# Optimization experiments

Hardware: AMD Instinct MI355X
Metric: run time of the kernel (lower is better)

The kernel has to match this reference:

```python
import jax, jax.numpy as jnp
import numpy as np

B, S, H = 4, 1024, 1024
NH, HD = 16, 64            # heads, head_dim (H = NH*HD)
E, K, I = 8, 2, 2048       # experts, top_k, moe_intermediate_size
CAP_FACTOR = 2.0
EPS_RMS = 1e-6
EPS_LN = 1e-6
SCALE = HD ** -0.5


def setup_inputs() -> dict:
    key = jax.random.key(0)
    ks = jax.random.split(key, 12)
    std = 0.02
    causal = jnp.where(jnp.tril(jnp.ones((S, S), bool)), 0.0, -1e9).astype(jnp.float32)
    return {
        "hidden_states": jax.random.normal(ks[0], (B, S, H), jnp.float32),
        "attn_mask": causal[None, None],                       # [1,1,S,S] additive
        "qw": jax.random.normal(ks[1], (H, H), jnp.float32) * std,
        "qb": jnp.zeros((H,), jnp.float32),
        "kw": jax.random.normal(ks[2], (H, H), jnp.float32) * std,
        "kb": jnp.zeros((H,), jnp.float32),
        "vw": jax.random.normal(ks[3], (H, H), jnp.float32) * std,
        "vb": jnp.zeros((H,), jnp.float32),
        "ow": jax.random.normal(ks[4], (H, H), jnp.float32) * std,
        "ob": jnp.zeros((H,), jnp.float32),
        "rms_w": jnp.ones((H,), jnp.float32),
        "gate_w": jax.random.normal(ks[5], (E, H), jnp.float32) * std,
        "w1": jax.random.normal(ks[6], (E, H, I), jnp.float32) * std,
        "b1": jnp.zeros((E, I), jnp.float32),
        "w2": jax.random.normal(ks[7], (E, I, H), jnp.float32) * std,
        "b2": jnp.zeros((E, H), jnp.float32),
        "ln_w": jnp.ones((H,), jnp.float32),
        "ln_b": jnp.zeros((H,), jnp.float32),
    }


def _rmsnorm(x, w):
    v = jnp.mean(x * x, axis=-1, keepdims=True)
    return w * (x * jax.lax.rsqrt(v + EPS_RMS))


def _layernorm(x, w, b):
    mu = jnp.mean(x, axis=-1, keepdims=True)
    var = jnp.mean((x - mu) ** 2, axis=-1, keepdims=True)
    return w * (x - mu) * jax.lax.rsqrt(var + EPS_LN) + b


def reference(hidden_states, attn_mask, qw, qb, kw, kb, vw, vb, ow, ob,
              rms_w, gate_w, w1, b1, w2, b2, ln_w, ln_b):
    x = hidden_states                                            # [B,S,H]
    # ---- attention (eval mode: dropout = identity) ----
    def heads(t):  # [B,S,H] -> [B,NH,S,HD]
        return t.reshape(B, S, NH, HD).transpose(0, 2, 1, 3)
    q = heads(x @ qw + qb)
    k = heads(x @ kw + kb)
    v = heads(x @ vw + vb)
    scores = jnp.einsum("bhqd,bhkd->bhqk", q, k) * SCALE + attn_mask
    p = jax.nn.softmax(scores.astype(jnp.float32), axis=-1).astype(q.dtype)
    ao = jnp.einsum("bhqk,bhkd->bhqd", p, v).transpose(0, 2, 1, 3).reshape(B, S, H)
    ao = ao @ ow + ob
    h = _rmsnorm(x + ao, rms_w)                                  # [B,S,H]
    # ---- MoE ----
    xf = h.reshape(-1, H)                                        # [T,H]
    T = B * S
    router_logits = xf.astype(jnp.float32) @ gate_w.T            # [T,E]
    probs = jax.nn.softmax(router_logits, axis=-1)
    tw, ti = jax.lax.top_k(probs, K)                             # [T,K]
    tw = tw / (jnp.sum(tw, axis=-1, keepdims=True) + 1e-20)      # norm_topk_prob
    tw = tw / K
    # capacity drop (deterministic cumulative-position variant; capacity_factor
    # chosen so no token overflows -> identical to the torch module in eval)
    capacity = int(B * S * K * CAP_FACTOR / E)
    flat = ti.reshape(-1)                                        # [T*K]
    oh = (flat[:, None] == jnp.arange(E)[None, :]).astype(jnp.int32)
    pos = jnp.cumsum(oh, axis=0) - oh                            # slot index per expert
    mypos = jnp.take_along_axis(pos, flat[:, None], axis=1)[:, 0].reshape(T, K)
    tw = jnp.where(mypos >= capacity, 0.0, tw).astype(xf.dtype)
    # dense per-expert FFN + weighted combine
    cw = jnp.sum(jax.nn.one_hot(ti, E, dtype=xf.dtype) * tw[..., None], axis=1)  # [T,E]
    h1 = jax.nn.gelu(jnp.einsum("th,ehi->tei", xf, w1) + b1, approximate=False)
    y = jnp.einsum("tei,eih->teh", h1, w2) + b2                  # [T,E,H]
    routed = jnp.einsum("te,teh->th", cw, y).reshape(B, S, H)
    # ---- final residual + LayerNorm ----
    out = _layernorm(h + routed, ln_w, ln_b)
    return out
```

## Files before the change

kernel.cpp:

```cpp
#include <hip/hip_runtime.h>

#define NB 4
#define SQL 1024
#define HDIM 1024
#define NHEAD 16
#define HEADD 64
#define NEXP 8
#define IDIM 2048
#define NTOK (NB*SQL)
#define CAPACITY 2048
#define ATT_SCALE 0.125f

typedef unsigned short u16;
typedef __attribute__((ext_vector_type(8))) short bf16x8;
typedef __attribute__((ext_vector_type(8))) unsigned short u16x8;
typedef __attribute__((ext_vector_type(4))) float f32x4;

__device__ __forceinline__ u16 f2bf(float f) {
  union { float f; unsigned u; } x; x.f = f;
  unsigned r = (x.u + 0x7fffu + ((x.u >> 16) & 1u)) >> 16;
  return (u16)r;
}
__device__ __forceinline__ float bf2f(u16 b) {
  union { unsigned u; float f; } x; x.u = ((unsigned)b) << 16;
  return x.f;
}
__device__ __forceinline__ float wave_sum(float v) {
#pragma unroll
  for (int off = 32; off > 0; off >>= 1) v += __shfl_xor(v, off);
  return v;
}
__device__ __forceinline__ void gload_lds16(const u16* g, u16* l) {
  __builtin_amdgcn_global_load_lds(
      (const __attribute__((address_space(1))) void*)g,
      (__attribute__((address_space(3))) void*)l, 16, 0, 0);
}

__global__ __launch_bounds__(256)
void cvt_bf16_kernel(const float* __restrict__ in, u16* __restrict__ out)
{
  size_t i = (size_t)blockIdx.x * 1024 + threadIdx.x * 4;
  float4 v = *(const float4*)&in[i];
  ushort4 o = {f2bf(v.x), f2bf(v.y), f2bf(v.z), f2bf(v.w)};
  *(ushort4*)&out[i] = o;
}

__global__ __launch_bounds__(256)
void transpose_cvt_kernel(const float* __restrict__ in, u16* __restrict__ out,
                          int R, int C)
{
  int e = blockIdx.z;
  const float* ine = in + (size_t)e * R * C;
  u16* oute = out + (size_t)e * R * C;
  __shared__ u16 Ts[32 * 34];
  int tx = threadIdx.x & 31, ty = threadIdx.x >> 5;
  int r0 = blockIdx.y * 32, c0 = blockIdx.x * 32;
#pragma unroll
  for (int qq = 0; qq < 4; ++qq) {
    int rr = ty + qq * 8;
    Ts[tx * 34 + rr] = f2bf(ine[(size_t)(r0 + rr) * C + c0 + tx]);
  }
  __syncthreads();
#pragma unroll
  for (int qq = 0; qq < 4; ++qq) {
    int cc = ty + qq * 8;
    oute[(size_t)(c0 + cc) * R + r0 + tx] = Ts[cc * 34 + tx];
  }
}

__global__ __launch_bounds__(256)
void qkv_mfma_kernel(const u16* __restrict__ xbf,
                     const u16* __restrict__ wqT, const u16* __restrict__ wkT,
                     const u16* __restrict__ wvT,
                     const float* __restrict__ bq, const float* __restrict__ bk,
                     const float* __restrict__ bv,
                     u16* __restrict__ q, u16* __restrict__ k, u16* __restrict__ v)
{
  int mode = blockIdx.z;
  const u16* BT   = (mode == 0) ? wqT : (mode == 1) ? wkT : wvT;
  const float* bia = (mode == 0) ? bq : (mode == 1) ? bk : bv;
  u16* dst         = (mode == 0) ? q : (mode == 1) ? k : v;
  int m0 = blockIdx.x * 128, n0 = blockIdx.y * 128;
  __shared__ __align__(16) u16 As0[128 * 64];
  __shared__ __align__(16) u16 As1[128 * 64];
  __shared__ __align__(16) u16 Bs0[128 * 64];
  __shared__ __align__(16) u16 Bs1[128 * 64];
  int tid = threadIdx.x;
  f32x4 acc[4][4];
#pragma unroll
  for (int i = 0; i < 4; ++i)
#pragma unroll
    for (int j = 0; j < 4; ++j) acc[i][j] = (f32x4){0.f, 0.f, 0.f, 0.f};
  int w = tid >> 6, l = tid & 63;
  int lr = l & 15, lq = l >> 4;
  int wm = (w & 1) * 64, wn = (w >> 1) * 64;
  const u16* aptr[4]; const u16* bptr[4];
#pragma unroll
  for (int p = 0; p < 4; ++p) {
    int flat = p * 256 + tid;
    int r = flat >> 3, c = flat & 7;
    int cs = (c ^ (r & 7)) * 8;
    aptr[p] = xbf + (size_t)(m0 + r) * HDIM + cs;
    bptr[p] = BT + (size_t)(n0 + r) * HDIM + cs;
  }
  auto STAGE = [&](u16* A, u16* B, int k0) {
#pragma unroll
    for (int p = 0; p < 4; ++p) {
      size_t o = (size_t)(p * 256 + w * 64) * 8;
      gload_lds16(aptr[p] + k0, A + o);
      gload_lds16(bptr[p] + k0, B + o);
    }
  };
  auto COMPUTE = [&](const u16* Ab, const u16* Bb) {
#pragma unroll
    for (int s = 0; s < 2; ++s) {
      bf16x8 af[4], bfv[4];
#pragma unroll
      for (int i = 0; i < 4; ++i) {
        int mloc = wm + i * 16 + lr;
        af[i]  = *(const bf16x8*)&Ab[(mloc * 8 + ((s * 4 + lq) ^ (mloc & 7))) * 8];
        int n = wn + i * 16 + lr;
        bfv[i] = *(const bf16x8*)&Bb[(n * 8 + ((s * 4 + lq) ^ (n & 7))) * 8];
      }
#pragma unroll
      for (int i = 0; i < 4; ++i)
#pragma unroll
        for (int j = 0; j < 4; ++j)
          acc[i][j] = __builtin_amdgcn_mfma_f32_16x16x32_bf16(af[i], bfv[j], acc[i][j], 0, 0, 0);
    }
  };
  const int NT = HDIM / 64;
  STAGE(As0, Bs0, 0);
  for (int t = 0; t < NT; t += 2) {
    __syncthreads();
    if (t + 1 < NT) STAGE(As1, Bs1, (t + 1) * 64);
    COMPUTE(As0, Bs0);
    __syncthreads();
    if (t + 2 < NT) STAGE(As0, Bs0, (t + 2) * 64);
    COMPUTE(As1, Bs1);
  }
#pragma unroll
  for (int i = 0; i < 4; ++i)
#pragma unroll
    for (int j = 0; j < 4; ++j) {
      int col = n0 + wn + j * 16 + lr;
      float bb = bia[col];
      int hh = col >> 6, d = col & 63;
#pragma unroll
      for (int r = 0; r < 4; ++r) {
        int tg = m0 + wm + i * 16 + lq * 4 + r;
        int bi = tg >> 10, s = tg & 1023;
        dst[((size_t)(bi * NHEAD + hh) * SQL + s) * HEADD + d] = f2bf(acc[i][j][r] + bb);
      }
    }
}

__global__ __launch_bounds__(256)
void proj_mfma_kernel(const u16* __restrict__ aobf, const u16* __restrict__ owT,
                      const float* __restrict__ ob, float* __restrict__ out)
{
  int m0 = blockIdx.x * 128, n0 = blockIdx.y * 128;
  __shared__ __align__(16) u16 As0[128 * 64];
  __shared__ __align__(16) u16 As1[128 * 64];
  __shared__ __align__(16) u16 Bs0[128 * 64];
  __shared__ __align__(16) u16 Bs1[128 * 64];
  int tid = threadIdx.x;
  f32x4 acc[4][4];
#pragma unroll
  for (int i = 0; i < 4; ++i)
#pragma unroll
    for (int j = 0; j < 4; ++j) acc[i][j] = (f32x4){0.f, 0.f, 0.f, 0.f};
  int w = tid >> 6, l = tid & 63;
  int lr = l & 15, lq = l >> 4;
  int wm = (w & 1) * 64, wn = (w >> 1) * 64;
  const u16* aptr[4]; const u16* bptr[4];
#pragma unroll
  for (int p = 0; p < 4; ++p) {
    int flat = p * 256 + tid;
    int r = flat >> 3, c = flat & 7;
    int cs = (c ^ (r & 7)) * 8;
    aptr[p] = aobf + (size_t)(m0 + r) * HDIM + cs;
    bptr[p] = owT + (size_t)(n0 + r) * HDIM + cs;
  }
  auto STAGE = [&](u16* A, u16* B, int k0) {
#pragma unroll
    for (int p = 0; p < 4; ++p) {
      size_t o = (size_t)(p * 256 + w * 64) * 8;
      gload_lds16(aptr[p] + k0, A + o);
      gload_lds16(bptr[p] + k0, B + o);
    }
  };
  auto COMPUTE = [&](const u16* Ab, const u16* Bb) {
#pragma unroll
    for (int s = 0; s < 2; ++s) {
      bf16x8 af[4], bfv[4];
#pragma unroll
      for (int i = 0; i < 4; ++i) {
        int mloc = wm + i * 16 + lr;
        af[i]  = *(const bf16x8*)&Ab[(mloc * 8 + ((s * 4 + lq) ^ (mloc & 7))) * 8];
        int n = wn + i * 16 + lr;
        bfv[i] = *(const bf16x8*)&Bb[(n * 8 + ((s * 4 + lq) ^ (n & 7))) * 8];
      }
#pragma unroll
      for (int i = 0; i < 4; ++i)
#pragma unroll
        for (int j = 0; j < 4; ++j)
          acc[i][j] = __builtin_amdgcn_mfma_f32_16x16x32_bf16(af[i], bfv[j], acc[i][j], 0, 0, 0);
    }
  };
  const int NT = HDIM / 64;
  STAGE(As0, Bs0, 0);
  for (int t = 0; t < NT; t += 2) {
    __syncthreads();
    if (t + 1 < NT) STAGE(As1, Bs1, (t + 1) * 64);
    COMPUTE(As0, Bs0);
    __syncthreads();
    if (t + 2 < NT) STAGE(As0, Bs0, (t + 2) * 64);
    COMPUTE(As1, Bs1);
  }
#pragma unroll
  for (int i = 0; i < 4; ++i)
#pragma unroll
    for (int j = 0; j < 4; ++j) {
      int col = n0 + wn + j * 16 + lr;
      float bb = ob[col];
#pragma unroll
      for (int r = 0; r < 4; ++r) {
        int tg = m0 + wm + i * 16 + lq * 4 + r;
        out[(size_t)tg * HDIM + col] = acc[i][j][r] + bb;
      }
    }
}

__global__ __launch_bounds__(256)
void attn_mfma_kernel(const u16* __restrict__ q, const u16* __restrict__ k,
                      const u16* __restrict__ v, u16* __restrict__ ao)
{
  __shared__ __align__(16) u16 VT[64 * 72];
  __shared__ __align__(16) u16 Pl[4][16 * 72];
  int bid = blockIdx.x;
  int bh = bid & 63;
  int qt = 15 - (bid >> 6);
  int q0 = qt * 64;
  int tid = threadIdx.x;
  int w = tid >> 6, l = tid & 63;
  int lr = l & 15, lq = l >> 4;

  const u16* qp = q + ((size_t)bh * SQL + q0 + w * 16 + lr) * HEADD + lq * 8;
  bf16x8 qf0 = *(const bf16x8*)qp;
  bf16x8 qf1 = *(const bf16x8*)(qp + 32);

  float mrow[4], lrow[4];
  f32x4 Ot[4];
#pragma unroll
  for (int r = 0; r < 4; ++r) { mrow[r] = -1e30f; lrow[r] = 0.f; }
#pragma unroll
  for (int j = 0; j < 4; ++j) Ot[j] = (f32x4){0.f, 0.f, 0.f, 0.f};

  int vkey = 2 * (l & 31);
  int vd0 = w * 16 + (l >> 5) * 8;

  for (int kb = 0; kb <= q0; kb += 64) {
    __syncthreads();
    {
      const u16* vp = v + ((size_t)bh * SQL + kb + vkey) * HEADD + vd0;
      u16x8 a = *(const u16x8*)vp;
      u16x8 b = *(const u16x8*)(vp + HEADD);
#pragma unroll
      for (int e = 0; e < 8; ++e) {
        ushort2 pr = {a[e], b[e]};
        *(ushort2*)&VT[(vd0 + e) * 72 + vkey] = pr;
      }
    }
    f32x4 sacc[4];
#pragma unroll
    for (int j = 0; j < 4; ++j) sacc[j] = (f32x4){0.f, 0.f, 0.f, 0.f};
    const u16* kp = k + ((size_t)bh * SQL + kb + lr) * HEADD + lq * 8;
#pragma unroll
    for (int j = 0; j < 4; ++j) {
      bf16x8 kf0 = *(const bf16x8*)(kp + (size_t)j * 16 * HEADD);
      bf16x8 kf1 = *(const bf16x8*)(kp + (size_t)j * 16 * HEADD + 32);
      sacc[j] = __builtin_amdgcn_mfma_f32_16x16x32_bf16(qf0, kf0, sacc[j], 0, 0, 0);
      sacc[j] = __builtin_amdgcn_mfma_f32_16x16x32_bf16(qf1, kf1, sacc[j], 0, 0, 0);
    }
    bool diag = (kb == q0);
    float pv[4][4];
#pragma unroll
    for (int r = 0; r < 4; ++r) {
      float sv[4];
      float rm = -1e30f;
#pragma unroll
      for (int j = 0; j < 4; ++j) {
        float s0 = sacc[j][r] * ATT_SCALE;
        if (diag && (j * 16 + lr) > (w * 16 + lq * 4 + r)) s0 = -1e30f;
        sv[j] = s0;
        rm = fmaxf(rm, s0);
      }
      rm = fmaxf(rm, __shfl_xor(rm, 1));
      rm = fmaxf(rm, __shfl_xor(rm, 2));
      rm = fmaxf(rm, __shfl_xor(rm, 4));
      rm = fmaxf(rm, __shfl_xor(rm, 8));
      float mnew = fmaxf(mrow[r], rm);
      float alpha = __expf(mrow[r] - mnew);
      mrow[r] = mnew;
      float rl = 0.f;
#pragma unroll
      for (int j = 0; j < 4; ++j) {
        float p = __expf(sv[j] - mnew);
        pv[j][r] = p;
        rl += p;
      }
      rl += __shfl_xor(rl, 1);
      rl += __shfl_xor(rl, 2);
      rl += __shfl_xor(rl, 4);
      rl += __shfl_xor(rl, 8);
      lrow[r] = lrow[r] * alpha + rl;
#pragma unroll
      for (int j2 = 0; j2 < 4; ++j2) Ot[j2][r] *= alpha;
    }
#pragma unroll
    for (int j = 0; j < 4; ++j)
#pragma unroll
      for (int r = 0; r < 4; ++r)
        Pl[w][(lq * 4 + r) * 72 + j * 16 + lr] = f2bf(pv[j][r]);
    __syncthreads();
    const u16* pbase = &Pl[w][lr * 72];
#pragma unroll
    for (int s = 0; s < 2; ++s) {
      bf16x8 pa = *(const bf16x8*)(pbase + s * 32 + lq * 8);
#pragma unroll
      for (int j2 = 0; j2 < 4; ++j2) {
        bf16x8 vb = *(const bf16x8*)&VT[(j2 * 16 + lr) * 72 + s * 32 + lq * 8];
        Ot[j2] = __builtin_amdgcn_mfma_f32_16x16x32_bf16(pa, vb, Ot[j2], 0, 0, 0);
      }
    }
  }
  int b = bh >> 4, hh = bh & 15;
#pragma unroll
  for (int r = 0; r < 4; ++r) {
    float invl = 1.0f / lrow[r];
    int row = q0 + w * 16 + lq * 4 + r;
#pragma unroll
    for (int j2 = 0; j2 < 4; ++j2)
      ao[((size_t)(b * SQL + row)) * HDIM + hh * HEADD + j2 * 16 + lr] =
          f2bf(Ot[j2][r] * invl);
  }
}

__global__ __launch_bounds__(256)
void rmsnorm_kernel(const float* __restrict__ x, const float* __restrict__ p,
                    const float* __restrict__ w, float* __restrict__ out,
                    u16* __restrict__ outbf)
{
  int t = blockIdx.x, tid = threadIdx.x;
  float4 xv = ((const float4*)(x + (size_t)t * HDIM))[tid];
  float4 pv = ((const float4*)(p + (size_t)t * HDIM))[tid];
  float4 s = {xv.x + pv.x, xv.y + pv.y, xv.z + pv.z, xv.w + pv.w};
  float ss = s.x * s.x + s.y * s.y + s.z * s.z + s.w * s.w;
  __shared__ float red[4];
  float wsv = wave_sum(ss);
  int wid = tid >> 6, l = tid & 63;
  if (l == 0) red[wid] = wsv;
  __syncthreads();
  float tot = red[0] + red[1] + red[2] + red[3];
  float inv = 1.0f / sqrtf(tot / (float)HDIM + 1e-6f);
  float4 wv = ((const float4*)w)[tid];
  float4 o = {s.x * inv * wv.x, s.y * inv * wv.y, s.z * inv * wv.z, s.w * inv * wv.w};
  ((float4*)(out + (size_t)t * HDIM))[tid] = o;
  ushort4 ob = {f2bf(o.x), f2bf(o.y), f2bf(o.z), f2bf(o.w)};
  ((ushort4*)(outbf + (size_t)t * HDIM))[tid] = ob;
}

__global__ __launch_bounds__(256)
void router_kernel(const float* __restrict__ h, const float* __restrict__ gw,
                   int* __restrict__ ti, float* __restrict__ tw)
{
  int wid = threadIdx.x >> 6, l = threadIdx.x & 63;
  int t = blockIdx.x * 4 + wid;
  const float* hr = h + (size_t)t * HDIM;
  float hv[16];
#pragma unroll
  for (int j = 0; j < 16; ++j) hv[j] = hr[l + 64 * j];
  float lg[NEXP];
#pragma unroll
  for (int e = 0; e < NEXP; ++e) {
    const float* g = gw + (size_t)e * HDIM;
    float p = 0.f;
#pragma unroll
    for (int j = 0; j < 16; ++j) p += hv[j] * g[l + 64 * j];
    lg[e] = wave_sum(p);
  }
  if (l == 0) {
    int i1 = 0; float m1 = lg[0];
#pragma unroll
    for (int e = 1; e < NEXP; ++e) if (lg[e] > m1) { m1 = lg[e]; i1 = e; }
    int i2 = 0; float m2 = -1e30f;
#pragma unroll
    for (int e = 0; e < NEXP; ++e) if (e != i1 && lg[e] > m2) { m2 = lg[e]; i2 = e; }
    float se = 0.f;
#pragma unroll
    for (int e = 0; e < NEXP; ++e) se += expf(lg[e] - m1);
    float p1 = 1.0f / se;
    float p2 = expf(m2 - m1) / se;
    float denom = p1 + p2 + 1e-20f;
    tw[t * 2]     = p1 / denom * 0.5f;
    tw[t * 2 + 1] = p2 / denom * 0.5f;
    ti[t * 2]     = i1;
    ti[t * 2 + 1] = i2;
  }
}

__global__ __launch_bounds__(1024)
void scan_kernel(const int* __restrict__ ti, int* __restrict__ eidx,
                 int* __restrict__ counts, int* __restrict__ slotmap,
                 int* __restrict__ ebase)
{
  __shared__ int wc[16][NEXP];
  __shared__ int wbase[16][NEXP];
  __shared__ int tot[NEXP];
  __shared__ int eb[NEXP];
  int tid = threadIdx.x;
  int w = tid >> 6, l = tid & 63;
  unsigned long long below = (l == 0) ? 0ull : ((~0ull) >> (64 - l));
  const int CH = (NTOK * 2) / 16;
  const int RND = CH / 64;
  int ev[RND];
  int myc[NEXP];
#pragma unroll
  for (int e = 0; e < NEXP; ++e) myc[e] = 0;
#pragma unroll
  for (int c2 = 0; c2 < RND; ++c2) {
    int f = w * CH + c2 * 64 + l;
    int e = ti[f];
    ev[c2] = e;
#pragma unroll
    for (int e0 = 0; e0 < NEXP; ++e0)
      myc[e0] += __popcll(__ballot(e == e0));
  }
  if (l == 0) {
#pragma unroll
    for (int e = 0; e < NEXP; ++e) wc[w][e] = myc[e];
  }
  __syncthreads();
  if (tid < NEXP) {
    int run = 0;
#pragma unroll
    for (int ww = 0; ww < 16; ++ww) { wbase[ww][tid] = run; run += wc[ww][tid]; }
    tot[tid] = run;
    counts[tid] = (run < CAPACITY) ? run : CAPACITY;
  }
  __syncthreads();
  if (tid == 0) {
    int run = 0;
#pragma unroll
    for (int e = 0; e < NEXP; ++e) {
      eb[e] = run;
      ebase[e] = run;
      int c = tot[e];
      run += (c < CAPACITY) ? c : CAPACITY;
    }
  }
  __syncthreads();
  int base[NEXP];
#pragma unroll
  for (int e = 0; e < NEXP; ++e) base[e] = wbase[w][e];
#pragma unroll
  for (int c2 = 0; c2 < RND; ++c2) {
    int f = w * CH + c2 * 64 + l;
    int e = ev[c2];
    int mypos = 0;
#pragma unroll
    for (int e0 = 0; e0 < NEXP; ++e0) {
      unsigned long long mm = __ballot(e == e0);
      if (e == e0) mypos = base[e0] + __popcll(mm & below);
      base[e0] += __popcll(mm);
    }
    int sm_;
    if (mypos < CAPACITY) {
      eidx[e * CAPACITY + mypos] = f >> 1;
      sm_ = eb[e] + mypos;
    } else sm_ = -1;
    slotmap[f] = sm_;
  }
}

__global__ __launch_bounds__(256)
void moe_gemm1_kernel(const u16* __restrict__ hbf, const u16* __restrict__ w1T,
                      const float* __restrict__ b1, const int* __restrict__ eidx,
                      const int* __restrict__ counts, const int* __restrict__ ebase,
                      u16* __restrict__ h1)
{
  int bid = blockIdx.x;
  int e = bid & 7;
  int idx = bid >> 3;
  int m0 = (idx & 15) * 128;
  int n0 = (idx >> 4) * 128;
  int cnt = counts[e];
  if (m0 >= cnt) return;
  int base = ebase[e];
  __shared__ __align__(16) u16 As0[128 * 64];
  __shared__ __align__(16) u16 As1[128 * 64];
  __shared__ __align__(16) u16 Bs0[128 * 64];
  __shared__ __align__(16) u16 Bs1[128 * 64];
  __shared__ int rowtok[128];
  int tid = threadIdx.x;
  if (tid < 128) {
    int r = m0 + tid;
    rowtok[tid] = (r < cnt) ? eidx[e * CAPACITY + r] : 0;
  }
  __syncthreads();
  const u16* BT = w1T + (size_t)e * IDIM * HDIM;
  f32x4 acc[4][4];
#pragma unroll
  for (int i = 0; i < 4; ++i)
#pragma unroll
    for (int j = 0; j < 4; ++j) acc[i][j] = (f32x4){0.f, 0.f, 0.f, 0.f};
  int w = tid >> 6, l = tid & 63;
  int lr = l & 15, lq = l >> 4;
  int wm = (w & 1) * 64, wn = (w >> 1) * 64;
  const u16* aptr[4]; const u16* bptr[4];
#pragma unroll
  for (int p = 0; p < 4; ++p) {
    int flat = p * 256 + tid;
    int r = flat >> 3, c = flat & 7;
    int cs = (c ^ (r & 7)) * 8;
    aptr[p] = hbf + (size_t)rowtok[r] * HDIM + cs;
    bptr[p] = BT + (size_t)(n0 + r) * HDIM + cs;
  }
  auto STAGE = [&](u16* A, u16* B, int k0) {
#pragma unroll
    for (int p = 0; p < 4; ++p) {
      size_t o = (size_t)(p * 256 + w * 64) * 8;
      gload_lds16(aptr[p] + k0, A + o);
      gload_lds16(bptr[p] + k0, B + o);
    }
  };
  auto COMPUTE = [&](const u16* Ab, const u16* Bb) {
#pragma unroll
    for (int s = 0; s < 2; ++s) {
      bf16x8 af[4], bfv[4];
#pragma unroll
      for (int i = 0; i < 4; ++i) {
        int mloc = wm + i * 16 + lr;
        af[i]  = *(const bf16x8*)&Ab[(mloc * 8 + ((s * 4 + lq) ^ (mloc & 7))) * 8];
        int n = wn + i * 16 + lr;
        bfv[i] = *(const bf16x8*)&Bb[(n * 8 + ((s * 4 + lq) ^ (n & 7))) * 8];
      }
#pragma unroll
      for (int i = 0; i < 4; ++i)
#pragma unroll
        for (int j = 0; j < 4; ++j)
          acc[i][j] = __builtin_amdgcn_mfma_f32_16x16x32_bf16(af[i], bfv[j], acc[i][j], 0, 0, 0);
    }
  };
  const int NT = HDIM / 64;
  STAGE(As0, Bs0, 0);
#pragma unroll 1
  for (int t = 0; t < NT; t += 2) {
    __builtin_amdgcn_s_barrier();
    __builtin_amdgcn_sched_barrier(0);
    if (t + 1 < NT) {
      STAGE(As1, Bs1, (t + 1) * 64);
      asm volatile("s_waitcnt vmcnt(8)" ::: "memory");
    } else {
      asm volatile("s_waitcnt vmcnt(0)" ::: "memory");
    }
    __builtin_amdgcn_sched_barrier(0);
    __builtin_amdgcn_s_barrier();
    __builtin_amdgcn_sched_barrier(0);
    COMPUTE(As0, Bs0);
    __builtin_amdgcn_s_barrier();
    __builtin_amdgcn_sched_barrier(0);
    if (t + 2 < NT) {
      STAGE(As0, Bs0, (t + 2) * 64);
      asm volatile("s_waitcnt vmcnt(8)" ::: "memory");
    } else {
      asm volatile("s_waitcnt vmcnt(0)" ::: "memory");
    }
    __builtin_amdgcn_sched_barrier(0);
    __builtin_amdgcn_s_barrier();
    __builtin_amdgcn_sched_barrier(0);
    COMPUTE(As1, Bs1);
  }
#pragma unroll
  for (int i = 0; i < 4; ++i)
#pragma unroll
    for (int j = 0; j < 4; ++j) {
      int col = n0 + wn + j * 16 + lr;
      float bb = b1[(size_t)e * IDIM + col];
#pragma unroll
      for (int r = 0; r < 4; ++r) {
        int rowl = m0 + wm + i * 16 + lq * 4 + r;
        if (rowl < cnt) {
          float y = acc[i][j][r] + bb;
          float g = 0.5f * y * (1.0f + erff(y * 0.70710678118654752f));
          h1[(size_t)(base + rowl) * IDIM + col] = f2bf(g);
        }
      }
    }
}

__global__ __launch_bounds__(256)
void moe_gemm2_kernel(const u16* __restrict__ h1, const u16* __restrict__ w2T,
                      const float* __restrict__ b2, const int* __restrict__ counts,
                      const int* __restrict__ ebase, u16* __restrict__ ybuf)
{
  int bid = blockIdx.x;
  int e = bid & 7;
  int idx = bid >> 3;
  int m0 = (idx & 15) * 128;
  int n0 = (idx >> 4) * 128;
  int cnt = counts[e];
  if (m0 >= cnt) return;
  int base = ebase[e];
  __shared__ __align__(16) u16 As0[128 * 64];
  __shared__ __align__(16) u16 As1[128 * 64];
  __shared__ __align__(16) u16 Bs0[128 * 64];
  __shared__ __align__(16) u16 Bs1[128 * 64];
  int tid = threadIdx.x;
  const u16* BT = w2T + (size_t)e * HDIM * IDIM;
  f32x4 acc[4][4];
#pragma unroll
  for (int i = 0; i < 4; ++i)
#pragma unroll
    for (int j = 0; j < 4; ++j) acc[i][j] = (f32x4){0.f, 0.f, 0.f, 0.f};
  int w = tid >> 6, l = tid & 63;
  int lr = l & 15, lq = l >> 4;
  int wm = (w & 1) * 64, wn = (w >> 1) * 64;
  const u16* aptr[4]; const u16* bptr[4];
#pragma unroll
  for (int p = 0; p < 4; ++p) {
    int flat = p * 256 + tid;
    int r = flat >> 3, c = flat & 7;
    int cs = (c ^ (r & 7)) * 8;
    int rowg = m0 + r;
    if (rowg >= cnt) rowg = cnt - 1;
    aptr[p] = h1 + (size_t)(base + rowg) * IDIM + cs;
    bptr[p] = BT + (size_t)(n0 + r) * IDIM + cs;
  }
  auto STAGE = [&](u16* A, u16* B, int k0) {
#pragma unroll
    for (int p = 0; p < 4; ++p) {
      size_t o = (size_t)(p * 256 + w * 64) * 8;
      gload_lds16(aptr[p] + k0, A + o);
      gload_lds16(bptr[p] + k0, B + o);
    }
  };
  auto COMPUTE = [&](const u16* Ab, const u16* Bb) {
#pragma unroll
    for (int s = 0; s < 2; ++s) {
      bf16x8 af[4], bfv[4];
#pragma unroll
      for (int i = 0; i < 4; ++i) {
        int mloc = wm + i * 16 + lr;
        af[i]  = *(const bf16x8*)&Ab[(mloc * 8 + ((s * 4 + lq) ^ (mloc & 7))) * 8];
        int n = wn + i * 16 + lr;
        bfv[i] = *(const bf16x8*)&Bb[(n * 8 + ((s * 4 + lq) ^ (n & 7))) * 8];
      }
#pragma unroll
      for (int i = 0; i < 4; ++i)
#pragma unroll
        for (int j = 0; j < 4; ++j)
          acc[i][j] = __builtin_amdgcn_mfma_f32_16x16x32_bf16(af[i], bfv[j], acc[i][j], 0, 0, 0);
    }
  };
  const int NT = IDIM / 64;
  STAGE(As0, Bs0, 0);
#pragma unroll 1
  for (int t = 0; t < NT; t += 2) {
    __builtin_amdgcn_s_barrier();
    __builtin_amdgcn_sched_barrier(0);
    if (t + 1 < NT) {
      STAGE(As1, Bs1, (t + 1) * 64);
      asm volatile("s_waitcnt vmcnt(8)" ::: "memory");
    } else {
      asm volatile("s_waitcnt vmcnt(0)" ::: "memory");
    }
    __builtin_amdgcn_sched_barrier(0);
    __builtin_amdgcn_s_barrier();
    __builtin_amdgcn_sched_barrier(0);
    COMPUTE(As0, Bs0);
    __builtin_amdgcn_s_barrier();
    __builtin_amdgcn_sched_barrier(0);
    if (t + 2 < NT) {
      STAGE(As0, Bs0, (t + 2) * 64);
      asm volatile("s_waitcnt vmcnt(8)" ::: "memory");
    } else {
      asm volatile("s_waitcnt vmcnt(0)" ::: "memory");
    }
    __builtin_amdgcn_sched_barrier(0);
    __builtin_amdgcn_s_barrier();
    __builtin_amdgcn_sched_barrier(0);
    COMPUTE(As1, Bs1);
  }
#pragma unroll
  for (int i = 0; i < 4; ++i)
#pragma unroll
    for (int j = 0; j < 4; ++j) {
      int col = n0 + wn + j * 16 + lr;
      float bb = b2[(size_t)e * HDIM + col];
#pragma unroll
      for (int r = 0; r < 4; ++r) {
        int rowl = m0 + wm + i * 16 + lq * 4 + r;
        if (rowl < cnt)
          ybuf[(size_t)(base + rowl) * HDIM + col] = f2bf(acc[i][j][r] + bb);
      }
    }
}

__global__ __launch_bounds__(256)
void final_kernel(const float* __restrict__ h, const u16* __restrict__ ybuf,
                  const int* __restrict__ slotmap, const float* __restrict__ tw,
                  const float* __restrict__ lnw, const float* __restrict__ lnb,
                  float* __restrict__ out)
{
  int t = blockIdx.x, tid = threadIdx.x;
  int s0 = slotmap[t * 2], s1 = slotmap[t * 2 + 1];
  float w0 = tw[t * 2], w1v = tw[t * 2 + 1];
  float4 hv = ((const float4*)(h + (size_t)t * HDIM))[tid];
  float vals[4] = {hv.x, hv.y, hv.z, hv.w};
  if (s0 >= 0) {
    const u16* yr = ybuf + (size_t)s0 * HDIM + tid * 4;
#pragma unroll
    for (int j = 0; j < 4; ++j) vals[j] += w0 * bf2f(yr[j]);
  }
  if (s1 >= 0) {
    const u16* yr = ybuf + (size_t)s1 * HDIM + tid * 4;
#pragma unroll
    for (int j = 0; j < 4; ++j) vals[j] += w1v * bf2f(yr[j]);
  }
  float s = vals[0] + vals[1] + vals[2] + vals[3];
  float q2 = vals[0] * vals[0] + vals[1] * vals[1] + vals[2] * vals[2] + vals[3] * vals[3];
  __shared__ float reds[4], redq[4];
  float wsv = wave_sum(s), wqv = wave_sum(q2);
  int wid = tid >> 6, l = tid & 63;
  if (l == 0) { reds[wid] = wsv; redq[wid] = wqv; }
  __syncthreads();
  float tot = reds[0] + reds[1] + reds[2] + reds[3];
  float totq = redq[0] + redq[1] + redq[2] + redq[3];
  float mu = tot / 1024.0f;
  float var = totq / 1024.0f - mu * mu;
  float inv = 1.0f / sqrtf(var + 1e-6f);
#pragma unroll
  for (int j = 0; j < 4; ++j) {
    int c = tid * 4 + j;
    out[(size_t)t * HDIM + c] = (vals[j] - mu) * inv * lnw[c] + lnb[c];
  }
}

extern "C" void kernel_launch(void* const* d_in, const int* in_sizes, int n_in,
                              void* d_out, int out_size, void* d_ws, size_t ws_size,
                              hipStream_t stream)
{
  const float* x      = (const float*)d_in[0];
  const float* qw     = (const float*)d_in[2];
  const float* qb     = (const float*)d_in[3];
  const float* kw     = (const float*)d_in[4];
  const float* kb     = (const float*)d_in[5];
  const float* vw     = (const float*)d_in[6];
  const float* vb     = (const float*)d_in[7];
  const float* ow     = (const float*)d_in[8];
  const float* ob     = (const float*)d_in[9];
  const float* rms_w  = (const float*)d_in[10];
  const float* gate_w = (const float*)d_in[11];
  const float* w1     = (const float*)d_in[12];
  const float* b1     = (const float*)d_in[13];
  const float* w2     = (const float*)d_in[14];
  const float* b2     = (const float*)d_in[15];
  const float* ln_w   = (const float*)d_in[16];
  const float* ln_b   = (const float*)d_in[17];

  char* ws = (char*)d_ws;
  const size_t MB = 1024ull * 1024ull;
  u16*   qbf    = (u16*)(ws + 0 * MB);
  u16*   kbf    = (u16*)(ws + 8 * MB);
  u16*   vbf    = (u16*)(ws + 16 * MB);
  u16*   aobf   = (u16*)(ws + 24 * MB);
  u16*   xbf    = (u16*)(ws + 32 * MB);
  u16*   wqT    = (u16*)(ws + 40 * MB);
  u16*   wkT    = (u16*)(ws + 42 * MB);
  u16*   wvT    = (u16*)(ws + 44 * MB);
  u16*   owT    = (u16*)(ws + 46 * MB);
  float* projbuf= (float*)(ws + 48 * MB);
  float* hbuf   = (float*)(ws + 64 * MB);
  u16*   hbf    = (u16*)(ws + 80 * MB);
  u16*   wT     = (u16*)(ws + 0 * MB);
  u16*   ybuf   = (u16*)(ws + 32 * MB);
  u16*   h1buf  = (u16*)(ws + 88 * MB);
  char*  sm     = ws + 120 * MB;
  int*   ti      = (int*)(sm);
  float* tw      = (float*)(sm + 32 * 1024);
  int*   eidx    = (int*)(sm + 64 * 1024);
  int*   slotmap = (int*)(sm + 128 * 1024);
  int*   counts  = (int*)(sm + 160 * 1024);
  int*   ebase   = (int*)(sm + 164 * 1024);
  bool   sepw2   = ws_size >= 156 * MB;
  u16*   w2T     = sepw2 ? (u16*)(ws + 124 * MB) : wT;

  cvt_bf16_kernel<<<NTOK, 256, 0, stream>>>(x, xbf);
  transpose_cvt_kernel<<<dim3(32, 32, 1), 256, 0, stream>>>(qw, wqT, HDIM, HDIM);
  transpose_cvt_kernel<<<dim3(32, 32, 1), 256, 0, stream>>>(kw, wkT, HDIM, HDIM);
  transpose_cvt_kernel<<<dim3(32, 32, 1), 256, 0, stream>>>(vw, wvT, HDIM, HDIM);
  transpose_cvt_kernel<<<dim3(32, 32, 1), 256, 0, stream>>>(ow, owT, HDIM, HDIM);
  qkv_mfma_kernel<<<dim3(NTOK / 128, HDIM / 128, 3), 256, 0, stream>>>(
      xbf, wqT, wkT, wvT, qb, kb, vb, qbf, kbf, vbf);
  attn_mfma_kernel<<<NB * NHEAD * (SQL / 64), 256, 0, stream>>>(qbf, kbf, vbf, aobf);
  proj_mfma_kernel<<<dim3(NTOK / 128, HDIM / 128), 256, 0, stream>>>(
      aobf, owT, ob, projbuf);
  rmsnorm_kernel<<<NTOK, 256, 0, stream>>>(x, projbuf, rms_w, hbuf, hbf);
  transpose_cvt_kernel<<<dim3(IDIM / 32, HDIM / 32, NEXP), 256, 0, stream>>>(
      w1, wT, HDIM, IDIM);
  if (sepw2)
    transpose_cvt_kernel<<<dim3(HDIM / 32, IDIM / 32, NEXP), 256, 0, stream>>>(
        w2, w2T, IDIM, HDIM);
  router_kernel<<<NTOK / 4, 256, 0, stream>>>(hbuf, gate_w, ti, tw);
  scan_kernel<<<1, 1024, 0, stream>>>(ti, eidx, counts, slotmap, ebase);
  moe_gemm1_kernel<<<dim3(NEXP * (CAPACITY / 128) * (IDIM / 128)), 256, 0, stream>>>(
      hbf, wT, b1, eidx, counts, ebase, h1buf);
  if (!sepw2)
    transpose_cvt_kernel<<<dim3(HDIM / 32, IDIM / 32, NEXP), 256, 0, stream>>>(
        w2, w2T, IDIM, HDIM);
  moe_gemm2_kernel<<<dim3(NEXP * (CAPACITY / 128) * (HDIM / 128)), 256, 0, stream>>>(
      h1buf, w2T, b2, counts, ebase, ybuf);
  final_kernel<<<NTOK, 256, 0, stream>>>(hbuf, ybuf, slotmap, tw, ln_w, ln_b,
                                         (float*)d_out);
}
```

Before: 547.0 us.

## Fuse router into RMSNorm, batch QKVO transposes, simplify MoE GEMM pipelines

The four QKV/O weight transpose launches become one batched launch, and router logits are now computed inside the RMSNorm kernel from shared memory, which removes a kernel launch and a re-read of hbuf. The MoE GEMM main loops also drop the hand-tuned barriers, sched_barriers and partial vmcnt waits in favour of plain __syncthreads and compiler-scheduled loads. That last change may weaken load/compute overlap in the largest kernels. The fused router now issues one block per token with only two experts per wave, instead of four tokens per block.

```diff
diff --git a/kernel.cpp b/kernel.cpp
--- a/kernel.cpp
+++ b/kernel.cpp
@@ -67,6 +67,31 @@
     oute[(size_t)(c0 + cc) * R + r0 + tx] = Ts[cc * 34 + tx];
   }
 }
+
+__global__ __launch_bounds__(256)
+void transpose_cvt4_kernel(const float* __restrict__ w0, const float* __restrict__ w1,
+                           const float* __restrict__ w2, const float* __restrict__ w3,
+                           u16* __restrict__ outbase)
+{
+  int z = blockIdx.z;
+  const float* ine = (z == 0) ? w0 : (z == 1) ? w1 : (z == 2) ? w2 : w3;
+  u16* oute = outbase + (size_t)z * HDIM * HDIM;
+  __shared__ u16 Ts[32 * 34];
+  int tx = threadIdx.x & 31, ty = threadIdx.x >> 5;
+  int r0 = blockIdx.y * 32, c0 = blockIdx.x * 32;
+#pragma unroll
+  for (int qq = 0; qq < 4; ++qq) {
+    int rr = ty + qq * 8;
+    Ts[tx * 34 + rr] = f2bf(ine[(size_t)(r0 + rr) * HDIM + c0 + tx]);
+  }
+  __syncthreads();
+#pragma unroll
+  for (int qq = 0; qq < 4; ++qq) {
+    int cc = ty + qq * 8;
+    oute[(size_t)(c0 + cc) * HDIM + r0 + tx] = Ts[cc * 34 + tx];
+  }
+}
+
 
 __global__ __launch_bounds__(256)
 void qkv_mfma_kernel(const u16* __restrict__ xbf,
@@ -348,9 +373,10 @@
 }
 
 __global__ __launch_bounds__(256)
-void rmsnorm_kernel(const float* __restrict__ x, const float* __restrict__ p,
-                    const float* __restrict__ w, float* __restrict__ out,
-                    u16* __restrict__ outbf)
+void rmsnorm_router_kernel(const float* __restrict__ x, const float* __restrict__ p,
+                           const float* __restrict__ w, const float* __restrict__ gw,
+                           float* __restrict__ out, u16* __restrict__ outbf,
+                           int* __restrict__ ti, float* __restrict__ tw)
 {
   int t = blockIdx.x, tid = threadIdx.x;
   float4 xv = ((const float4*)(x + (size_t)t * HDIM))[tid];
@@ -358,6 +384,8 @@
   float4 s = {xv.x + pv.x, xv.y + pv.y, xv.z + pv.z, xv.w + pv.w};
   float ss = s.x * s.x + s.y * s.y + s.z * s.z + s.w * s.w;
   __shared__ float red[4];
+  __shared__ float hsm[HDIM];
+  __shared__ float lgs[NEXP];
   float wsv = wave_sum(ss);
   int wid = tid >> 6, l = tid & 63;
   if (l == 0) red[wid] = wsv;
@@ -369,28 +397,23 @@
   ((float4*)(out + (size_t)t * HDIM))[tid] = o;
   ushort4 ob = {f2bf(o.x), f2bf(o.y), f2bf(o.z), f2bf(o.w)};
   ((ushort4*)(outbf + (size_t)t * HDIM))[tid] = ob;
-}
-
-__global__ __launch_bounds__(256)
-void router_kernel(const float* __restrict__ h, const float* __restrict__ gw,
-                   int* __restrict__ ti, float* __restrict__ tw)
-{
-  int wid = threadIdx.x >> 6, l = threadIdx.x & 63;
-  int t = blockIdx.x * 4 + wid;
-  const float* hr = h + (size_t)t * HDIM;
-  float hv[16];
-#pragma unroll
-  for (int j = 0; j < 16; ++j) hv[j] = hr[l + 64 * j];
-  float lg[NEXP];
-#pragma unroll
-  for (int e = 0; e < NEXP; ++e) {
+  *(float4*)&hsm[tid * 4] = o;
+  __syncthreads();
+#pragma unroll
+  for (int ee = 0; ee < 2; ++ee) {
+    int e = wid * 2 + ee;
     const float* g = gw + (size_t)e * HDIM;
-    float p = 0.f;
-#pragma unroll
-    for (int j = 0; j < 16; ++j) p += hv[j] * g[l + 64 * j];
-    lg[e] = wave_sum(p);
-  }
-  if (l == 0) {
+    float pacc = 0.f;
+#pragma unroll
+    for (int j = 0; j < 16; ++j) pacc += hsm[l + 64 * j] * g[l + 64 * j];
+    float sv = wave_sum(pacc);
+    if (l == 0) lgs[e] = sv;
+  }
+  __syncthreads();
+  if (tid == 0) {
+    float lg[NEXP];
+#pragma unroll
+    for (int e = 0; e < NEXP; ++e) lg[e] = lgs[e];
     int i1 = 0; float m1 = lg[0];
 #pragma unroll
     for (int e = 1; e < NEXP; ++e) if (lg[e] > m1) { m1 = lg[e]; i1 = e; }
@@ -555,31 +578,12 @@
   };
   const int NT = HDIM / 64;
   STAGE(As0, Bs0, 0);
-#pragma unroll 1
   for (int t = 0; t < NT; t += 2) {
-    __builtin_amdgcn_s_barrier();
-    __builtin_amdgcn_sched_barrier(0);
-    if (t + 1 < NT) {
-      STAGE(As1, Bs1, (t + 1) * 64);
-      asm volatile("s_waitcnt vmcnt(8)" ::: "memory");
-    } else {
-      asm volatile("s_waitcnt vmcnt(0)" ::: "memory");
-    }
-    __builtin_amdgcn_sched_barrier(0);
-    __builtin_amdgcn_s_barrier();
-    __builtin_amdgcn_sched_barrier(0);
+    __syncthreads();
+    if (t + 1 < NT) STAGE(As1, Bs1, (t + 1) * 64);
     COMPUTE(As0, Bs0);
-    __builtin_amdgcn_s_barrier();
-    __builtin_amdgcn_sched_barrier(0);
-    if (t + 2 < NT) {
-      STAGE(As0, Bs0, (t + 2) * 64);
-      asm volatile("s_waitcnt vmcnt(8)" ::: "memory");
-    } else {
-      asm volatile("s_waitcnt vmcnt(0)" ::: "memory");
-    }
-    __builtin_amdgcn_sched_barrier(0);
-    __builtin_amdgcn_s_barrier();
-    __builtin_amdgcn_sched_barrier(0);
+    __syncthreads();
+    if (t + 2 < NT) STAGE(As0, Bs0, (t + 2) * 64);
     COMPUTE(As1, Bs1);
   }
 #pragma unroll
@@ -666,31 +670,12 @@
   };
   const int NT = IDIM / 64;
   STAGE(As0, Bs0, 0);
-#pragma unroll 1
   for (int t = 0; t < NT; t += 2) {
-    __builtin_amdgcn_s_barrier();
-    __builtin_amdgcn_sched_barrier(0);
-    if (t + 1 < NT) {
-      STAGE(As1, Bs1, (t + 1) * 64);
-      asm volatile("s_waitcnt vmcnt(8)" ::: "memory");
-    } else {
-      asm volatile("s_waitcnt vmcnt(0)" ::: "memory");
-    }
-    __builtin_amdgcn_sched_barrier(0);
-    __builtin_amdgcn_s_barrier();
-    __builtin_amdgcn_sched_barrier(0);
+    __syncthreads();
+    if (t + 1 < NT) STAGE(As1, Bs1, (t + 1) * 64);
     COMPUTE(As0, Bs0);
-    __builtin_amdgcn_s_barrier();
-    __builtin_amdgcn_sched_barrier(0);
-    if (t + 2 < NT) {
-      STAGE(As0, Bs0, (t + 2) * 64);
-      asm volatile("s_waitcnt vmcnt(8)" ::: "memory");
-    } else {
-      asm volatile("s_waitcnt vmcnt(0)" ::: "memory");
-    }
-    __builtin_amdgcn_sched_barrier(0);
-    __builtin_amdgcn_s_barrier();
-    __builtin_amdgcn_sched_barrier(0);
+    __syncthreads();
+    if (t + 2 < NT) STAGE(As0, Bs0, (t + 2) * 64);
     COMPUTE(As1, Bs1);
   }
 #pragma unroll
@@ -777,10 +762,11 @@
   u16*   vbf    = (u16*)(ws + 16 * MB);
   u16*   aobf   = (u16*)(ws + 24 * MB);
   u16*   xbf    = (u16*)(ws + 32 * MB);
-  u16*   wqT    = (u16*)(ws + 40 * MB);
-  u16*   wkT    = (u16*)(ws + 42 * MB);
-  u16*   wvT    = (u16*)(ws + 44 * MB);
-  u16*   owT    = (u16*)(ws + 46 * MB);
+  u16*   wqkvoT = (u16*)(ws + 40 * MB);
+  u16*   wqT    = wqkvoT;
+  u16*   wkT    = wqkvoT + 1 * HDIM * HDIM;
+  u16*   wvT    = wqkvoT + 2 * HDIM * HDIM;
+  u16*   owT    = wqkvoT + 3 * HDIM * HDIM;
   float* projbuf= (float*)(ws + 48 * MB);
   float* hbuf   = (float*)(ws + 64 * MB);
   u16*   hbf    = (u16*)(ws + 80 * MB);
@@ -798,22 +784,19 @@
   u16*   w2T     = sepw2 ? (u16*)(ws + 124 * MB) : wT;
 
   cvt_bf16_kernel<<<NTOK, 256, 0, stream>>>(x, xbf);
-  transpose_cvt_kernel<<<dim3(32, 32, 1), 256, 0, stream>>>(qw, wqT, HDIM, HDIM);
-  transpose_cvt_kernel<<<dim3(32, 32, 1), 256, 0, stream>>>(kw, wkT, HDIM, HDIM);
-  transpose_cvt_kernel<<<dim3(32, 32, 1), 256, 0, stream>>>(vw, wvT, HDIM, HDIM);
-  transpose_cvt_kernel<<<dim3(32, 32, 1), 256, 0, stream>>>(ow, owT, HDIM, HDIM);
+  transpose_cvt4_kernel<<<dim3(32, 32, 4), 256, 0, stream>>>(qw, kw, vw, ow, wqkvoT);
   qkv_mfma_kernel<<<dim3(NTOK / 128, HDIM / 128, 3), 256, 0, stream>>>(
       xbf, wqT, wkT, wvT, qb, kb, vb, qbf, kbf, vbf);
   attn_mfma_kernel<<<NB * NHEAD * (SQL / 64), 256, 0, stream>>>(qbf, kbf, vbf, aobf);
   proj_mfma_kernel<<<dim3(NTOK / 128, HDIM / 128), 256, 0, stream>>>(
       aobf, owT, ob, projbuf);
-  rmsnorm_kernel<<<NTOK, 256, 0, stream>>>(x, projbuf, rms_w, hbuf, hbf);
+  rmsnorm_router_kernel<<<NTOK, 256, 0, stream>>>(x, projbuf, rms_w, gate_w,
+                                                  hbuf, hbf, ti, tw);
   transpose_cvt_kernel<<<dim3(IDIM / 32, HDIM / 32, NEXP), 256, 0, stream>>>(
       w1, wT, HDIM, IDIM);
   if (sepw2)
     transpose_cvt_kernel<<<dim3(HDIM / 32, IDIM / 32, NEXP), 256, 0, stream>>>(
         w2, w2T, IDIM, HDIM);
-  router_kernel<<<NTOK / 4, 256, 0, stream>>>(hbuf, gate_w, ti, tw);
   scan_kernel<<<1, 1024, 0, stream>>>(ti, eidx, counts, slotmap, ebase);
   moe_gemm1_kernel<<<dim3(NEXP * (CAPACITY / 128) * (IDIM / 128)), 256, 0, stream>>>(
       hbf, wT, b1, eidx, counts, ebase, h1buf);
```

Result: faster. 528.3 us (-3.4%).
